# Performance work log

Measured on AMD Instinct MI355X. Metric: run time of the kernel, lower is better.

## Reference

```python
import jax
import jax.numpy as jnp
from jax import lax
import numpy as np

BATCH, SEQ, STATES = 64, 4096, 64


def setup_inputs() -> dict:
    key = jax.random.key(0)
    k1, k2, k3, k4 = jax.random.split(key, 4)
    scores = jax.random.normal(k1, (BATCH, SEQ, STATES), dtype=jnp.float32)
    transition = jax.random.normal(k2, (STATES, STATES), dtype=jnp.float32)
    source = jax.random.uniform(k3, (STATES,), dtype=jnp.float32)
    sink = jax.random.uniform(k4, (STATES,), dtype=jnp.float32)
    return {"scores": scores, "transition": transition, "source": source, "sink": sink}


def reference(scores, transition, source, sink):
    # Linear-chain CRF log-partition (forward algorithm in log space).
    # scores: (B, T, S) emission scores; transition: (S, S) [from, to].
    B, T, S = scores.shape
    # t == 0: original code logsumexps a broadcast-identical axis of size S,
    # which adds a constant log(S) -- reproduced here for bit-faithful math.
    score0 = source[None, :] + scores[:, 0] + jnp.log(jnp.asarray(S, scores.dtype))  # (B, S)

    def step(alpha, s_t):
        # alpha: (B, S) log-scores over previous state; s_t: (B, S) emissions at t
        new = jax.nn.logsumexp(alpha[:, :, None] + transition[None, :, :], axis=1) + s_t
        return new, None

    # scan over time: (T-1, B, S)
    alpha_final, _ = lax.scan(step, score0, jnp.swapaxes(scores[:, 1:], 0, 1))
    return jax.nn.logsumexp(alpha_final + sink[None, :], axis=1)  # (B,)
```

## Files before the change

### kernel.cpp

```cpp
#include <hip/hip_runtime.h>
#include <cstdint>


#define B_    64
#define T_    4096
#define S_    64
#define L_    15
#define NC_   273
#define WPB_  18
#define CPB_  288
#define LOG2E 1.44269504088896340736f

typedef float  f32x4  __attribute__((ext_vector_type(4)));
typedef __bf16 bf16x8 __attribute__((ext_vector_type(8)));
union U4B { uint4 u; bf16x8 b; };

__global__ __launch_bounds__(64, 3) void crf_phase1(
    const float* __restrict__ scores,
    const float* __restrict__ transition,
    float* __restrict__ Ybuf, float* __restrict__ Zbuf, float* __restrict__ Lz)
{
    __shared__ float tb[16][68];
    const int wid  = blockIdx.x;
    const bool bwd = wid >= (B_ * WPB_);
    const int wl   = bwd ? wid - B_ * WPB_ : wid;
    const int b    = wl / WPB_, wg = wl % WPB_;
    const int lane = threadIdx.x, g = lane >> 4, l = lane & 15;

    bf16x8 BE[2][4];
    #pragma unroll
    for (int kb = 0; kb < 2; ++kb)
    #pragma unroll
    for (int nt = 0; nt < 4; ++nt) {
        bf16x8 t;
        #pragma unroll
        for (int dd = 0; dd < 4; ++dd) {
            int k0 = 32 * kb + 8 * g + 2 * dd, n = 16 * nt + l;
            float e0, e1;
            if (!bwd) { e0 = transition[k0 * 64 + n]; e1 = transition[(k0 + 1) * 64 + n]; }
            else      { e0 = transition[n * 64 + k0]; e1 = transition[n * 64 + k0 + 1]; }
            t[2 * dd]     = (__bf16)exp2f(e0 * LOG2E);
            t[2 * dd + 1] = (__bf16)exp2f(e1 * LOG2E);
        }
        BE[kb][nt] = t;
    }

    int cl = 16 * wg + l; if (cl > NC_ - 1) cl = NC_ - 1;
    const float* ap = scores + ((size_t)b * T_ + L_ * cl + (bwd ? L_ : 0)) * S_ + 8 * g;

    f32x4 acc[4];
    f32x4 ring[3][4];
    int   Lt[4] = {0, 0, 0, 0};

    auto ldq = [&](int idx, f32x4* q) {
        const float* p = ap + (ptrdiff_t)idx * S_;
        q[0] = *(const f32x4*)p;        q[1] = *(const f32x4*)(p + 4);
        q[2] = *(const f32x4*)(p + 32); q[3] = *(const f32x4*)(p + 36);
    };
    auto mfma8 = [&](bf16x8 A0, bf16x8 A1) {
        #pragma unroll
        for (int nt = 0; nt < 4; ++nt) {
            f32x4 z4 = {0.f, 0.f, 0.f, 0.f};
            z4      = __builtin_amdgcn_mfma_f32_16x16x32_bf16(A0, BE[0][nt], z4, 0, 0, 0);
            acc[nt] = __builtin_amdgcn_mfma_f32_16x16x32_bf16(A1, BE[1][nt], z4, 0, 0, 0);
        }
    };
    auto renorm = [&]() {
        #pragma unroll
        for (int r = 0; r < 4; ++r) {
            float m = fmaxf(fmaxf(acc[0][r], acc[1][r]), fmaxf(acc[2][r], acc[3][r]));
            m = fmaxf(m, __shfl_xor(m, 1, 64));
            m = fmaxf(m, __shfl_xor(m, 2, 64));
            m = fmaxf(m, __shfl_xor(m, 4, 64));
            m = fmaxf(m, __shfl_xor(m, 8, 64));
            int ex = (int)(__float_as_uint(m) >> 23) - 127;
            float sc = __uint_as_float((unsigned)(127 - ex) << 23);
            Lt[r] += ex;
            #pragma unroll
            for (int nt = 0; nt < 4; ++nt) acc[nt][r] *= sc;
        }
    };
    auto xposeA = [&](const f32x4& c0, const f32x4& c1,
                      const f32x4& c2, const f32x4& c3, bf16x8& A0, bf16x8& A1) {
        #pragma unroll
        for (int nt = 0; nt < 4; ++nt)
            #pragma unroll
            for (int r = 0; r < 4; ++r)
                tb[4 * g + r][16 * nt + l] = acc[nt][r];
        __builtin_amdgcn_s_waitcnt(0xC07F);
        __builtin_amdgcn_wave_barrier();
        const float* rowp = &tb[l][8 * g];
        f32x4 x0 = *(const f32x4*)rowp;
        f32x4 x1 = *(const f32x4*)(rowp + 4);
        f32x4 x2 = *(const f32x4*)(rowp + 32);
        f32x4 x3 = *(const f32x4*)(rowp + 36);
        #pragma unroll
        for (int d = 0; d < 4; ++d) {
            A0[d]     = (__bf16)(x0[d] * exp2f(c0[d] * LOG2E));
            A0[d + 4] = (__bf16)(x1[d] * exp2f(c1[d] * LOG2E));
            A1[d]     = (__bf16)(x2[d] * exp2f(c2[d] * LOG2E));
            A1[d + 4] = (__bf16)(x3[d] * exp2f(c3[d] * LOG2E));
        }
    };

    if (!bwd) {
        ldq(1, ring[0]); ldq(2, ring[1]); ldq(3, ring[2]);
        { U4B t; t.u = make_uint4(0x3F803F80u, 0x3F803F80u, 0x3F803F80u, 0x3F803F80u);
          mfma8(t.b, t.b); }
        #pragma unroll
        for (int tt = 1; tt < L_; ++tt) {
            f32x4* q = ring[(tt - 1) % 3];
            f32x4 c0 = q[0], c1 = q[1], c2 = q[2], c3 = q[3];
            if (tt + 3 <= L_ - 1) ldq(tt + 3, ring[(tt - 1) % 3]);
            bf16x8 A0, A1;
            xposeA(c0, c1, c2, c3, A0, A1);
            mfma8(A0, A1);
            if ((tt & 3) == 3) renorm();
        }
        float* yb = Ybuf + ((size_t)(b * WPB_ + wg) << 10);
        #pragma unroll
        for (int nt = 0; nt < 4; ++nt)
            *(f32x4*)(yb + ((nt * 64 + lane) << 2)) = acc[nt];
    } else {
        ldq(0, ring[0]); ldq(-1, ring[1]); ldq(-2, ring[2]);
        {
            f32x4* q = ring[0];
            bf16x8 A0, A1;
            #pragma unroll
            for (int d = 0; d < 4; ++d) {
                A0[d]     = (__bf16)exp2f(q[0][d] * LOG2E);
                A0[d + 4] = (__bf16)exp2f(q[1][d] * LOG2E);
                A1[d]     = (__bf16)exp2f(q[2][d] * LOG2E);
                A1[d + 4] = (__bf16)exp2f(q[3][d] * LOG2E);
            }
            mfma8(A0, A1);
            ldq(-3, ring[0]);
        }
        #pragma unroll
        for (int i = 1; i < L_; ++i) {
            f32x4* q = ring[i % 3];
            f32x4 c0 = q[0], c1 = q[1], c2 = q[2], c3 = q[3];
            if (i + 3 <= L_ - 1) ldq(-(i + 3), ring[i % 3]);
            bf16x8 A0, A1;
            xposeA(c0, c1, c2, c3, A0, A1);
            mfma8(A0, A1);
            if ((i & 3) == 3) renorm();
        }
        float* zb = Zbuf + ((size_t)(b * WPB_ + wg) << 10);
        #pragma unroll
        for (int nt = 0; nt < 4; ++nt)
            *(f32x4*)(zb + ((nt * 64 + lane) << 2)) = acc[nt];
        if (l == 0) {
            #pragma unroll
            for (int r = 0; r < 4; ++r)
                Lz[b * CPB_ + 16 * wg + 4 * g + r] = (float)Lt[r];
        }
    }
}

__global__ __launch_bounds__(512) void crf_phase2(
    const float* __restrict__ scores, const float* __restrict__ source,
    const float* __restrict__ sink,
    const float* __restrict__ Ybuf, const float* __restrict__ Zbuf,
    const float* __restrict__ Lz, float* __restrict__ out)
{
    __shared__ float part[8];
    const int b = blockIdx.x;
    const int wv = threadIdx.x >> 6, lane = threadIdx.x & 63;
    const int q = lane >> 4, l = lane & 15;
    float acc = 0.f;

    for (int wg = wv; wg < WPB_; wg += 8) {
        const float* Yb = Ybuf + ((size_t)(b * WPB_ + wg) << 10);
        const float* Zb = Zbuf + ((size_t)(b * WPB_ + wg) << 10);
        f32x4 y[4], z[4];
        #pragma unroll
        for (int nt = 0; nt < 4; ++nt) {
            y[nt] = *(const f32x4*)(Yb + ((nt * 64 + lane) << 2));
            z[nt] = *(const f32x4*)(Zb + ((nt * 64 + lane) << 2));
        }
        float E2[4][4];
        #pragma unroll
        for (int r = 0; r < 4; ++r) {
            int c = 16 * wg + 4 * q + r; int cc = c < NC_ ? c : NC_ - 1;
            const float* er = scores + ((size_t)b * T_ + (size_t)15 * cc + 15) * S_;
            #pragma unroll
            for (int nt = 0; nt < 4; ++nt)
                E2[r][nt] = exp2f(er[16 * nt + l] * LOG2E);
        }
        float zn3[4];
        #pragma unroll
        for (int nt = 0; nt < 4; ++nt) zn3[nt] = __shfl(z[nt][0], lane + 16, 64);
        if (q == 3 && wg + 1 < WPB_) {
            const float* Zn = Zbuf + ((size_t)(b * WPB_ + wg + 1) << 10);
            #pragma unroll
            for (int nt = 0; nt < 4; ++nt) zn3[nt] = Zn[(nt * 64 + l) << 2];
        }
        float esk[4];
        #pragma unroll
        for (int nt = 0; nt < 4; ++nt) esk[nt] = exp2f(sink[16 * nt + l] * LOG2E);

        #pragma unroll
        for (int r = 0; r < 4; ++r) {
            int c = 16 * wg + 4 * q + r;
            float p = 0.f, qs = 0.f;
            #pragma unroll
            for (int nt = 0; nt < 4; ++nt) {
                float zz = (r < 3) ? z[nt][r + 1] : zn3[nt];
                if (c == NC_ - 1) zz = esk[nt];
                float ye = y[nt][r] * E2[r][nt];
                p  += ye * zz;
                qs += ye;
            }
            #pragma unroll
            for (int m = 1; m <= 8; m <<= 1) {
                p  += __shfl_xor(p, m, 64);
                qs += __shfl_xor(qs, m, 64);
            }
            if (l == 0 && c < NC_)
                acc += log2f(p) - log2f(qs) + Lz[b * CPB_ + c];
        }
        if (wg == 0 && q == 0) {
            float s0 = 0.f;
            #pragma unroll
            for (int nt = 0; nt < 4; ++nt) {
                float a0 = exp2f((source[16 * nt + l]
                                  + scores[(size_t)b * T_ * S_ + 16 * nt + l]) * LOG2E);
                s0 += a0 * z[nt][0];
            }
            #pragma unroll
            for (int m = 1; m <= 8; m <<= 1) s0 += __shfl_xor(s0, m, 64);
            if (l == 0) acc += log2f(s0);
        }
    }
    #pragma unroll
    for (int m = 32; m >= 1; m >>= 1) acc += __shfl_xor(acc, m, 64);
    if (lane == 0) part[wv] = acc;
    __syncthreads();
    if (threadIdx.x == 0) {
        float s = 0.f;
        #pragma unroll
        for (int i = 0; i < 8; ++i) s += part[i];
        out[b] = 0.6931471805599453f * s + 4.158883083359672f;
    }
}

extern "C" void kernel_launch(void* const* d_in, const int* in_sizes, int n_in,
                              void* d_out, int out_size, void* d_ws, size_t ws_size,
                              hipStream_t stream) {
    (void)in_sizes; (void)n_in; (void)out_size; (void)ws_size;
    const float* scores     = (const float*)d_in[0];
    const float* transition = (const float*)d_in[1];
    const float* source     = (const float*)d_in[2];
    const float* sink       = (const float*)d_in[3];
    float* out = (float*)d_out;

    float* Ybuf = (float*)d_ws;
    float* Zbuf = Ybuf + (size_t)B_ * WPB_ * 1024;
    float* Lz   = Zbuf + (size_t)B_ * WPB_ * 1024;

    hipLaunchKernelGGL(crf_phase1, dim3(2 * B_ * WPB_), dim3(64), 0, stream,
                       scores, transition, Ybuf, Zbuf, Lz);
    hipLaunchKernelGGL(crf_phase2, dim3(B_), dim3(512), 0, stream,
                       scores, source, sink, Ybuf, Zbuf, Lz, out);
}
```

Baseline: 125.3 us.

## Shorten chunk length and split phase-2 reduction across one wave per group

Chunk length drops from 15 to 9 steps, giving 455 chunks and 29 wave-groups per batch, so phase 1 launches more, shorter waves with a shorter serial dependency chain. Phase 2 now runs one 64-thread block per (batch, group) and writes partial sums to a buffer instead of looping 8 waves per batch. A new tiny phase-3 kernel sums the partials per batch. The cost is more workspace traffic, an extra kernel launch, and more renormalisation and boundary work from the larger number of chunks.

After: 128.7 us. +2.7%, slower.

```diff
diff --git a/kernel.cpp b/kernel.cpp
--- a/kernel.cpp
+++ b/kernel.cpp
@@ -5,10 +5,10 @@
 #define B_    64
 #define T_    4096
 #define S_    64
-#define L_    15
-#define NC_   273
-#define WPB_  18
-#define CPB_  288
+#define L_    9
+#define NC_   455
+#define WPB_  29
+#define CPB_  464
 #define LOG2E 1.44269504088896340736f
 
 typedef float  f32x4  __attribute__((ext_vector_type(4)));
@@ -158,91 +158,92 @@
     }
 }
 
-__global__ __launch_bounds__(512) void crf_phase2(
+__global__ __launch_bounds__(64) void crf_phase2(
     const float* __restrict__ scores, const float* __restrict__ source,
     const float* __restrict__ sink,
     const float* __restrict__ Ybuf, const float* __restrict__ Zbuf,
-    const float* __restrict__ Lz, float* __restrict__ out)
+    const float* __restrict__ Lz, float* __restrict__ Pbuf)
 {
-    __shared__ float part[8];
-    const int b = blockIdx.x;
-    const int wv = threadIdx.x >> 6, lane = threadIdx.x & 63;
+    const int bw = blockIdx.x;
+    const int b = bw / WPB_, wg = bw % WPB_;
+    const int lane = threadIdx.x;
     const int q = lane >> 4, l = lane & 15;
     float acc = 0.f;
 
-    for (int wg = wv; wg < WPB_; wg += 8) {
-        const float* Yb = Ybuf + ((size_t)(b * WPB_ + wg) << 10);
-        const float* Zb = Zbuf + ((size_t)(b * WPB_ + wg) << 10);
-        f32x4 y[4], z[4];
+    const float* Yb = Ybuf + ((size_t)bw << 10);
+    const float* Zb = Zbuf + ((size_t)bw << 10);
+    f32x4 y[4], z[4];
+    #pragma unroll
+    for (int nt = 0; nt < 4; ++nt) {
+        y[nt] = *(const f32x4*)(Yb + ((nt * 64 + lane) << 2));
+        z[nt] = *(const f32x4*)(Zb + ((nt * 64 + lane) << 2));
+    }
+    float E2[4][4];
+    #pragma unroll
+    for (int r = 0; r < 4; ++r) {
+        int c = 16 * wg + 4 * q + r; int cc = c < NC_ ? c : NC_ - 1;
+        const float* er = scores + ((size_t)b * T_ + (size_t)L_ * cc + L_) * S_;
+        #pragma unroll
+        for (int nt = 0; nt < 4; ++nt)
+            E2[r][nt] = exp2f(er[16 * nt + l] * LOG2E);
+    }
+    float zn3[4];
+    #pragma unroll
+    for (int nt = 0; nt < 4; ++nt) zn3[nt] = __shfl(z[nt][0], lane + 16, 64);
+    if (q == 3 && wg + 1 < WPB_) {
+        const float* Zn = Zbuf + (((size_t)bw + 1) << 10);
+        #pragma unroll
+        for (int nt = 0; nt < 4; ++nt) zn3[nt] = Zn[(nt * 64 + l) << 2];
+    }
+    float esk[4];
+    #pragma unroll
+    for (int nt = 0; nt < 4; ++nt) esk[nt] = exp2f(sink[16 * nt + l] * LOG2E);
+
+    #pragma unroll
+    for (int r = 0; r < 4; ++r) {
+        int c = 16 * wg + 4 * q + r;
+        float p = 0.f, qs = 0.f;
         #pragma unroll
         for (int nt = 0; nt < 4; ++nt) {
-            y[nt] = *(const f32x4*)(Yb + ((nt * 64 + lane) << 2));
-            z[nt] = *(const f32x4*)(Zb + ((nt * 64 + lane) << 2));
-        }
-        float E2[4][4];
-        #pragma unroll
-        for (int r = 0; r < 4; ++r) {
-            int c = 16 * wg + 4 * q + r; int cc = c < NC_ ? c : NC_ - 1;
-            const float* er = scores + ((size_t)b * T_ + (size_t)15 * cc + 15) * S_;
-            #pragma unroll
-            for (int nt = 0; nt < 4; ++nt)
-                E2[r][nt] = exp2f(er[16 * nt + l] * LOG2E);
-        }
-        float zn3[4];
-        #pragma unroll
-        for (int nt = 0; nt < 4; ++nt) zn3[nt] = __shfl(z[nt][0], lane + 16, 64);
-        if (q == 3 && wg + 1 < WPB_) {
-            const float* Zn = Zbuf + ((size_t)(b * WPB_ + wg + 1) << 10);
-            #pragma unroll
-            for (int nt = 0; nt < 4; ++nt) zn3[nt] = Zn[(nt * 64 + l) << 2];
-        }
-        float esk[4];
-        #pragma unroll
-        for (int nt = 0; nt < 4; ++nt) esk[nt] = exp2f(sink[16 * nt + l] * LOG2E);
-
-        #pragma unroll
-        for (int r = 0; r < 4; ++r) {
-            int c = 16 * wg + 4 * q + r;
-            float p = 0.f, qs = 0.f;
-            #pragma unroll
-            for (int nt = 0; nt < 4; ++nt) {
-                float zz = (r < 3) ? z[nt][r + 1] : zn3[nt];
-                if (c == NC_ - 1) zz = esk[nt];
-                float ye = y[nt][r] * E2[r][nt];
-                p  += ye * zz;
-                qs += ye;
-            }
-            #pragma unroll
-            for (int m = 1; m <= 8; m <<= 1) {
-                p  += __shfl_xor(p, m, 64);
-                qs += __shfl_xor(qs, m, 64);
-            }
-            if (l == 0 && c < NC_)
-                acc += log2f(p) - log2f(qs) + Lz[b * CPB_ + c];
-        }
-        if (wg == 0 && q == 0) {
-            float s0 = 0.f;
-            #pragma unroll
-            for (int nt = 0; nt < 4; ++nt) {
-                float a0 = exp2f((source[16 * nt + l]
-                                  + scores[(size_t)b * T_ * S_ + 16 * nt + l]) * LOG2E);
-                s0 += a0 * z[nt][0];
-            }
-            #pragma unroll
-            for (int m = 1; m <= 8; m <<= 1) s0 += __shfl_xor(s0, m, 64);
-            if (l == 0) acc += log2f(s0);
-        }
+            float zz = (r < 3) ? z[nt][r + 1] : zn3[nt];
+            if (c == NC_ - 1) zz = esk[nt];
+            float ye = y[nt][r] * E2[r][nt];
+            p  += ye * zz;
+            qs += ye;
+        }
+        #pragma unroll
+        for (int m = 1; m <= 8; m <<= 1) {
+            p  += __shfl_xor(p, m, 64);
+            qs += __shfl_xor(qs, m, 64);
+        }
+        if (l == 0 && c < NC_)
+            acc += log2f(p) - log2f(qs) + Lz[b * CPB_ + c];
+    }
+    if (wg == 0 && q == 0) {
+        float s0 = 0.f;
+        #pragma unroll
+        for (int nt = 0; nt < 4; ++nt) {
+            float a0 = exp2f((source[16 * nt + l]
+                              + scores[(size_t)b * T_ * S_ + 16 * nt + l]) * LOG2E);
+            s0 += a0 * z[nt][0];
+        }
+        #pragma unroll
+        for (int m = 1; m <= 8; m <<= 1) s0 += __shfl_xor(s0, m, 64);
+        if (l == 0) acc += log2f(s0);
     }
     #pragma unroll
     for (int m = 32; m >= 1; m >>= 1) acc += __shfl_xor(acc, m, 64);
-    if (lane == 0) part[wv] = acc;
-    __syncthreads();
-    if (threadIdx.x == 0) {
-        float s = 0.f;
-        #pragma unroll
-        for (int i = 0; i < 8; ++i) s += part[i];
-        out[b] = 0.6931471805599453f * s + 4.158883083359672f;
-    }
+    if (lane == 0) Pbuf[bw] = acc;
+}
+
+__global__ __launch_bounds__(64) void crf_phase3(
+    const float* __restrict__ Pbuf, float* __restrict__ out)
+{
+    const int b = threadIdx.x;
+    float s = 0.f;
+    #pragma unroll
+    for (int i = 0; i < WPB_; ++i) s += Pbuf[b * WPB_ + i];
+    out[b] = 0.6931471805599453f * s + 4.158883083359672f;
 }
 
 extern "C" void kernel_launch(void* const* d_in, const int* in_sizes, int n_in,
@@ -258,9 +259,11 @@
     float* Ybuf = (float*)d_ws;
     float* Zbuf = Ybuf + (size_t)B_ * WPB_ * 1024;
     float* Lz   = Zbuf + (size_t)B_ * WPB_ * 1024;
+    float* Pbuf = Lz   + (size_t)B_ * CPB_;
 
     hipLaunchKernelGGL(crf_phase1, dim3(2 * B_ * WPB_), dim3(64), 0, stream,
                        scores, transition, Ybuf, Zbuf, Lz);
-    hipLaunchKernelGGL(crf_phase2, dim3(B_), dim3(512), 0, stream,
-                       scores, source, sink, Ybuf, Zbuf, Lz, out);
-}
+    hipLaunchKernelGGL(crf_phase2, dim3(B_ * WPB_), dim3(64), 0, stream,
+                       scores, source, sink, Ybuf, Zbuf, Lz, Pbuf);
+    hipLaunchKernelGGL(crf_phase3, dim3(1), dim3(64), 0, stream, Pbuf, out);
+}
```

## Fuse forward/backward chunk waves into 4-wave blocks with in-block combine via LDS

Applied to the files above, without the earlier changes.

Shortens chunk length from 15 to 9 steps, which raises the number of chunks to 455 and shortens the serial recurrence per wave. Forward and backward waves for two chunk groups now share a 256-thread block, so the Y/Z combine happens in shared memory instead of through global Y/Z buffers and a second heavy pass. Only the per-block boundary vectors and partial sums go to a tiny reduce kernel. The trade-off is more chunks (more boundary work, more bf16 renormalization points), larger LDS use per block, and lower occupancy per block.

After: 141.8 us. 1.13x slower.

```diff
diff --git a/kernel.cpp b/kernel.cpp
--- a/kernel.cpp
+++ b/kernel.cpp
@@ -5,27 +5,50 @@
 #define B_    64
 #define T_    4096
 #define S_    64
-#define L_    15
-#define NC_   273
-#define WPB_  18
-#define CPB_  288
+#define L_    9
+#define NC_   455
+#define WPB_  30
+#define BPB_  15
 #define LOG2E 1.44269504088896340736f
 
 typedef float  f32x4  __attribute__((ext_vector_type(4)));
 typedef __bf16 bf16x8 __attribute__((ext_vector_type(8)));
 union U4B { uint4 u; bf16x8 b; };
 
-__global__ __launch_bounds__(64, 3) void crf_phase1(
+__global__ __launch_bounds__(256, 4) void crf_fused(
     const float* __restrict__ scores,
     const float* __restrict__ transition,
-    float* __restrict__ Ybuf, float* __restrict__ Zbuf, float* __restrict__ Lz)
+    const float* __restrict__ source, const float* __restrict__ sink,
+    float* __restrict__ zfirst,
+    float* __restrict__ wbuf,
+    float* __restrict__ Ltlast,
+    float* __restrict__ partial)
 {
-    __shared__ float tb[16][68];
-    const int wid  = blockIdx.x;
-    const bool bwd = wid >= (B_ * WPB_);
-    const int wl   = bwd ? wid - B_ * WPB_ : wid;
-    const int b    = wl / WPB_, wg = wl % WPB_;
-    const int lane = threadIdx.x, g = lane >> 4, l = lane & 15;
+    __shared__ float tb[4][16][68];
+    __shared__ float ys[32][64];
+    __shared__ float zs[32][64];
+    __shared__ float Ltz[32];
+    __shared__ float part[16];
+
+    const int j  = blockIdx.x % BPB_;
+    const int b  = blockIdx.x / BPB_;
+    const int wv = threadIdx.x >> 6;
+    const bool bwd = wv >= 2;
+    const int wg = 2 * j + (wv & 1);
+    const int lane = threadIdx.x & 63, g = lane >> 4, l = lane & 15;
+
+    int cl = 16 * wg + l; if (cl > NC_ - 1) cl = NC_ - 1;
+    const float* ap = scores + ((size_t)b * T_ + L_ * cl + (bwd ? L_ : 0)) * S_ + 8 * g;
+
+    f32x4 acc[4];
+    f32x4 ring[3][4];
+    int   Lt[4] = {0, 0, 0, 0};
+
+    auto ldq = [&](int idx, f32x4* q) {
+        const float* p = ap + (ptrdiff_t)idx * S_;
+        q[0] = *(const f32x4*)p;        q[1] = *(const f32x4*)(p + 4);
+        q[2] = *(const f32x4*)(p + 32); q[3] = *(const f32x4*)(p + 36);
+    };
 
     bf16x8 BE[2][4];
     #pragma unroll
@@ -45,18 +68,6 @@
         BE[kb][nt] = t;
     }
 
-    int cl = 16 * wg + l; if (cl > NC_ - 1) cl = NC_ - 1;
-    const float* ap = scores + ((size_t)b * T_ + L_ * cl + (bwd ? L_ : 0)) * S_ + 8 * g;
-
-    f32x4 acc[4];
-    f32x4 ring[3][4];
-    int   Lt[4] = {0, 0, 0, 0};
-
-    auto ldq = [&](int idx, f32x4* q) {
-        const float* p = ap + (ptrdiff_t)idx * S_;
-        q[0] = *(const f32x4*)p;        q[1] = *(const f32x4*)(p + 4);
-        q[2] = *(const f32x4*)(p + 32); q[3] = *(const f32x4*)(p + 36);
-    };
     auto mfma8 = [&](bf16x8 A0, bf16x8 A1) {
         #pragma unroll
         for (int nt = 0; nt < 4; ++nt) {
@@ -86,10 +97,10 @@
         for (int nt = 0; nt < 4; ++nt)
             #pragma unroll
             for (int r = 0; r < 4; ++r)
-                tb[4 * g + r][16 * nt + l] = acc[nt][r];
+                tb[wv][4 * g + r][16 * nt + l] = acc[nt][r];
         __builtin_amdgcn_s_waitcnt(0xC07F);
         __builtin_amdgcn_wave_barrier();
-        const float* rowp = &tb[l][8 * g];
+        const float* rowp = &tb[wv][l][8 * g];
         f32x4 x0 = *(const f32x4*)rowp;
         f32x4 x1 = *(const f32x4*)(rowp + 4);
         f32x4 x2 = *(const f32x4*)(rowp + 32);
@@ -117,10 +128,11 @@
             mfma8(A0, A1);
             if ((tt & 3) == 3) renorm();
         }
-        float* yb = Ybuf + ((size_t)(b * WPB_ + wg) << 10);
         #pragma unroll
         for (int nt = 0; nt < 4; ++nt)
-            *(f32x4*)(yb + ((nt * 64 + lane) << 2)) = acc[nt];
+            #pragma unroll
+            for (int r = 0; r < 4; ++r)
+                ys[16 * (wv & 1) + 4 * g + r][16 * nt + l] = acc[nt][r];
     } else {
         ldq(0, ring[0]); ldq(-1, ring[1]); ldq(-2, ring[2]);
         {
@@ -146,101 +158,98 @@
             mfma8(A0, A1);
             if ((i & 3) == 3) renorm();
         }
-        float* zb = Zbuf + ((size_t)(b * WPB_ + wg) << 10);
         #pragma unroll
         for (int nt = 0; nt < 4; ++nt)
-            *(f32x4*)(zb + ((nt * 64 + lane) << 2)) = acc[nt];
+            #pragma unroll
+            for (int r = 0; r < 4; ++r)
+                zs[16 * (wv & 1) + 4 * g + r][16 * nt + l] = acc[nt][r];
         if (l == 0) {
             #pragma unroll
             for (int r = 0; r < 4; ++r)
-                Lz[b * CPB_ + 16 * wg + 4 * g + r] = (float)Lt[r];
-        }
-    }
-}
-
-__global__ __launch_bounds__(512) void crf_phase2(
-    const float* __restrict__ scores, const float* __restrict__ source,
-    const float* __restrict__ sink,
-    const float* __restrict__ Ybuf, const float* __restrict__ Zbuf,
-    const float* __restrict__ Lz, float* __restrict__ out)
-{
-    __shared__ float part[8];
-    const int b = blockIdx.x;
-    const int wv = threadIdx.x >> 6, lane = threadIdx.x & 63;
-    const int q = lane >> 4, l = lane & 15;
-    float acc = 0.f;
-
-    for (int wg = wv; wg < WPB_; wg += 8) {
-        const float* Yb = Ybuf + ((size_t)(b * WPB_ + wg) << 10);
-        const float* Zb = Zbuf + ((size_t)(b * WPB_ + wg) << 10);
-        f32x4 y[4], z[4];
-        #pragma unroll
-        for (int nt = 0; nt < 4; ++nt) {
-            y[nt] = *(const f32x4*)(Yb + ((nt * 64 + lane) << 2));
-            z[nt] = *(const f32x4*)(Zb + ((nt * 64 + lane) << 2));
-        }
-        float E2[4][4];
-        #pragma unroll
-        for (int r = 0; r < 4; ++r) {
-            int c = 16 * wg + 4 * q + r; int cc = c < NC_ ? c : NC_ - 1;
-            const float* er = scores + ((size_t)b * T_ + (size_t)15 * cc + 15) * S_;
-            #pragma unroll
-            for (int nt = 0; nt < 4; ++nt)
-                E2[r][nt] = exp2f(er[16 * nt + l] * LOG2E);
-        }
-        float zn3[4];
-        #pragma unroll
-        for (int nt = 0; nt < 4; ++nt) zn3[nt] = __shfl(z[nt][0], lane + 16, 64);
-        if (q == 3 && wg + 1 < WPB_) {
-            const float* Zn = Zbuf + ((size_t)(b * WPB_ + wg + 1) << 10);
-            #pragma unroll
-            for (int nt = 0; nt < 4; ++nt) zn3[nt] = Zn[(nt * 64 + l) << 2];
-        }
-        float esk[4];
-        #pragma unroll
-        for (int nt = 0; nt < 4; ++nt) esk[nt] = exp2f(sink[16 * nt + l] * LOG2E);
-
-        #pragma unroll
-        for (int r = 0; r < 4; ++r) {
-            int c = 16 * wg + 4 * q + r;
-            float p = 0.f, qs = 0.f;
-            #pragma unroll
-            for (int nt = 0; nt < 4; ++nt) {
-                float zz = (r < 3) ? z[nt][r + 1] : zn3[nt];
-                if (c == NC_ - 1) zz = esk[nt];
-                float ye = y[nt][r] * E2[r][nt];
-                p  += ye * zz;
-                qs += ye;
+                Ltz[16 * (wv & 1) + 4 * g + r] = (float)Lt[r];
+        }
+    }
+    __syncthreads();
+
+    if (wv == 0) zfirst[((size_t)(b * BPB_ + j)) * 64 + lane] = zs[0][lane];
+
+    const int q = g;
+    float myterm = 0.f;
+    #pragma unroll
+    for (int h = 0; h < 2; ++h) {
+        const int m = 8 * wv + 2 * q + h;
+        const int c = 32 * j + m;
+        const int cc = c < NC_ ? c : NC_ - 1;
+        const float* er = scores + ((size_t)b * T_ + (size_t)L_ * (cc + 1)) * S_;
+        float ye[4], pp = 0.f, qs = 0.f;
+        #pragma unroll
+        for (int k = 0; k < 4; ++k) {
+            ye[k] = ys[m][16 * k + l] * exp2f(er[16 * k + l] * LOG2E);
+            float zz = (c == NC_ - 1) ? exp2f(sink[16 * k + l] * LOG2E)
+                                      : zs[(m + 1) & 31][16 * k + l];
+            pp += ye[k] * zz;
+            qs += ye[k];
+        }
+        #pragma unroll
+        for (int mm = 1; mm <= 8; mm <<= 1) {
+            pp += __shfl_xor(pp, mm, 64);
+            qs += __shfl_xor(qs, mm, 64);
+        }
+        if (m == 31) {
+            if (c < NC_ - 1) {
+                #pragma unroll
+                for (int k = 0; k < 4; ++k)
+                    wbuf[((size_t)(b * BPB_ + j)) * 64 + 16 * k + l] = ye[k];
+                if (l == 0) Ltlast[b * BPB_ + j] = Ltz[31];
             }
-            #pragma unroll
-            for (int m = 1; m <= 8; m <<= 1) {
-                p  += __shfl_xor(p, m, 64);
-                qs += __shfl_xor(qs, m, 64);
-            }
-            if (l == 0 && c < NC_)
-                acc += log2f(p) - log2f(qs) + Lz[b * CPB_ + c];
-        }
-        if (wg == 0 && q == 0) {
-            float s0 = 0.f;
-            #pragma unroll
-            for (int nt = 0; nt < 4; ++nt) {
-                float a0 = exp2f((source[16 * nt + l]
-                                  + scores[(size_t)b * T_ * S_ + 16 * nt + l]) * LOG2E);
-                s0 += a0 * z[nt][0];
-            }
-            #pragma unroll
-            for (int m = 1; m <= 8; m <<= 1) s0 += __shfl_xor(s0, m, 64);
-            if (l == 0) acc += log2f(s0);
-        }
-    }
-    #pragma unroll
-    for (int m = 32; m >= 1; m >>= 1) acc += __shfl_xor(acc, m, 64);
-    if (lane == 0) part[wv] = acc;
+        } else if (c < NC_ && l == 0) {
+            myterm += log2f(pp) - log2f(qs) + Ltz[m];
+        }
+    }
+    if (j == 0 && wv == 0 && q == 0) {
+        float s0 = 0.f;
+        #pragma unroll
+        for (int k = 0; k < 4; ++k) {
+            float a0 = exp2f((source[16 * k + l]
+                              + scores[(size_t)b * T_ * S_ + 16 * k + l]) * LOG2E);
+            s0 += a0 * zs[0][16 * k + l];
+        }
+        #pragma unroll
+        for (int mm = 1; mm <= 8; mm <<= 1) s0 += __shfl_xor(s0, mm, 64);
+        if (l == 0) myterm += log2f(s0);
+    }
+    if (l == 0) part[4 * wv + q] = myterm;
     __syncthreads();
     if (threadIdx.x == 0) {
         float s = 0.f;
         #pragma unroll
-        for (int i = 0; i < 8; ++i) s += part[i];
+        for (int i = 0; i < 16; ++i) s += part[i];
+        partial[b * BPB_ + j] = s;
+    }
+}
+
+__global__ __launch_bounds__(64) void crf_reduce(
+    const float* __restrict__ zfirst, const float* __restrict__ wbuf,
+    const float* __restrict__ Ltlast, const float* __restrict__ partial,
+    float* __restrict__ out)
+{
+    const int b = blockIdx.x;
+    const int lane = threadIdx.x;
+    float acc = 0.f;
+    for (int jj = 0; jj < BPB_ - 1; ++jj) {
+        float w  = wbuf  [((size_t)(b * BPB_ + jj)) * 64 + lane];
+        float zf = zfirst[((size_t)(b * BPB_ + jj + 1)) * 64 + lane];
+        float pp = w * zf, qs = w;
+        #pragma unroll
+        for (int mm = 1; mm <= 32; mm <<= 1) {
+            pp += __shfl_xor(pp, mm, 64);
+            qs += __shfl_xor(qs, mm, 64);
+        }
+        if (lane == 0) acc += log2f(pp) - log2f(qs) + Ltlast[b * BPB_ + jj];
+    }
+    if (lane == 0) {
+        float s = acc;
+        for (int jj = 0; jj < BPB_; ++jj) s += partial[b * BPB_ + jj];
         out[b] = 0.6931471805599453f * s + 4.158883083359672f;
     }
 }
@@ -255,12 +264,14 @@
     const float* sink       = (const float*)d_in[3];
     float* out = (float*)d_out;
 
-    float* Ybuf = (float*)d_ws;
-    float* Zbuf = Ybuf + (size_t)B_ * WPB_ * 1024;
-    float* Lz   = Zbuf + (size_t)B_ * WPB_ * 1024;
-
-    hipLaunchKernelGGL(crf_phase1, dim3(2 * B_ * WPB_), dim3(64), 0, stream,
-                       scores, transition, Ybuf, Zbuf, Lz);
-    hipLaunchKernelGGL(crf_phase2, dim3(B_), dim3(512), 0, stream,
-                       scores, source, sink, Ybuf, Zbuf, Lz, out);
+    float* zfirst  = (float*)d_ws;
+    float* wbuf    = zfirst + (size_t)B_ * BPB_ * 64;
+    float* Ltlast  = wbuf   + (size_t)B_ * BPB_ * 64;
+    float* partial = Ltlast + (size_t)B_ * BPB_;
+
+    hipLaunchKernelGGL(crf_fused, dim3(B_ * BPB_), dim3(256), 0, stream,
+                       scores, transition, source, sink,
+                       zfirst, wbuf, Ltlast, partial);
+    hipLaunchKernelGGL(crf_reduce, dim3(B_), dim3(64), 0, stream,
+                       zfirst, wbuf, Ltlast, partial, out);
 }
```
